# Optimization experiments

Hardware: AMD Instinct MI355X
Metric: run time of the kernel (lower is better)

Reference implementation:

```python
import jax, jax.numpy as jnp
import numpy as np

NFFT = 4_194_304
NMODES = 2
NTAPS = 101
GAMMA = 0.0016567  # [/W/m]
DZ = 80000.0       # [m]


def setup_inputs() -> dict:
    key = jax.random.key(0)
    k1, k2, k3 = jax.random.split(key, 3)
    xr = jax.random.normal(k1, (NFFT, NMODES), dtype=jnp.float32)
    xi = jax.random.normal(k2, (NFFT, NMODES), dtype=jnp.float32)
    # fconv1d kernel: [ntaps, in_features=Nmodes, out_features=Nmodes] (lecun_normal-ish scale)
    W = jax.random.normal(k3, (NTAPS, NMODES, NMODES), dtype=jnp.float32) / np.sqrt(NTAPS * NMODES)
    b = jnp.zeros((NMODES,), dtype=jnp.float32)
    power = jnp.zeros((1,), dtype=jnp.float32)  # 0 dBm
    return {"xr": xr, "xi": xi, "W": W, "b": b, "power": power}


def reference(xr, xi, W, b, power):
    # P = |x|^2, shape [Nfft, Nmodes]
    P = xr * xr + xi * xi
    # valid 1D conv over time: [Nfft, Nmodes] -> [Nfft - ntaps + 1, Nmodes]
    phi = jax.lax.conv_general_dilated(
        P[None],            # [1, Nfft, Nmodes]
        W,                  # [ntaps, in, out]
        window_strides=(1,),
        padding='VALID',
        dimension_numbers=('NWC', 'WIO', 'NWC'),
    )[0] + b                # [Nfft - ntaps + 1, Nmodes]

    nmodes = xr.shape[-1]
    scale = 0.001 * 10.0 ** (power[0] / 10.0) / nmodes  # dBm -> W, per mode
    n0 = NTAPS // 2
    x = (xr + 1j * xi)[n0:xr.shape[0] - n0]  # valid-conv aligned slice
    y = x * jnp.exp(-1j * phi * (GAMMA * scale * DZ))
    return y
```

## Files before the change

### kernel.cpp

```cpp
#include <hip/hip_runtime.h>
#include <hip/hip_bf16.h>

#define NFFT   4194304
#define NMODES 2
#define NTAPS  101
#define NVALID (NFFT - NTAPS + 1)
#define N0     (NTAPS / 2)

constexpr int BLOCK = 256;
constexpr int TILE  = 2048;
constexpr int NT    = (NVALID + TILE - 1) / TILE;
constexpr int WIN   = 2176;
constexpr int NCH   = WIN / 2;
constexpr int NM    = 15;
constexpr int TBW   = 272;

constexpr int OXA = 0;
constexpr int OXB = 4352;
constexpr int OPL = 8704;
constexpr int OBT = 10880;
constexpr int LWORDS = 11152;

typedef __attribute__((ext_vector_type(8)))  short short8;
typedef __attribute__((ext_vector_type(16))) float float16;

static __device__ __forceinline__ unsigned short f2bf(float x) {
    __hip_bfloat16 h = __float2bfloat16(x);
    return *reinterpret_cast<unsigned short*>(&h);
}
static __device__ __forceinline__ unsigned pk(float e0, float e1) {
    return (unsigned)f2bf(e0) | ((unsigned)f2bf(e1) << 16);
}
static __device__ __forceinline__ int swz(int s) {
    return s ^ (((s >> 5) & 7) << 2);
}
static __device__ __forceinline__ void gl16(const float4* g, unsigned* l) {
    __builtin_amdgcn_global_load_lds(
        (const __attribute__((address_space(1))) void*)g,
        (__attribute__((address_space(3))) void*)l, 16, 0, 0);
}

__global__ __launch_bounds__(BLOCK, 3) void nl_kernel(
    const float* __restrict__ xa,
    const float* __restrict__ xb,
    const float* __restrict__ W,  const float* __restrict__ b,
    const float* __restrict__ power, unsigned* __restrict__ out)
{
    __shared__ __align__(16) unsigned lds[LWORDS];
    unsigned* const xaR = lds + OXA;
    unsigned* const xbR = lds + OXB;
    unsigned* const Pl  = lds + OPL;
    unsigned* const Bt  = lds + OBT;

    const int tid  = threadIdx.x;
    const int lane = tid & 63;
    const int wid  = tid >> 6;
    const int colc = lane & 31;
    const int h    = lane >> 5;
    const int cs   = colc >> 1;
    const int o    = colc & 1;
    const int r    = colc;

    const int tile_start = blockIdx.x * TILE;
    const int ts2        = tile_start >> 1;

    const float4* __restrict__ xa4 = reinterpret_cast<const float4*>(xa);
    const float4* __restrict__ xb4 = reinterpret_cast<const float4*>(xb);
    #pragma unroll
    for (int k = 0; k < 4; ++k) {
        const int c  = tid + 256 * k;
        const int cc = min(ts2 + c, NFFT / 2 - 1);
        gl16(xa4 + cc, &xaR[4 * c]);
        gl16(xb4 + cc, &xbR[4 * c]);
    }
    if (tid < 64) {
        const int c  = tid + 1024;
        const int cc = min(ts2 + c, NFFT / 2 - 1);
        gl16(xa4 + cc, &xaR[4 * c]);
        gl16(xb4 + cc, &xbR[4 * c]);
    }

    __builtin_amdgcn_sched_barrier(0);

    {
        const float4* __restrict__ Wt = reinterpret_cast<const float4*>(W);
        #pragma unroll
        for (int idx = tid; idx < TBW; idx += BLOCK) {
            const int t  = (idx >> 1) - 15;
            const int oo = idx & 1;
            const bool ok = (unsigned)t <= 100u;
            const float4 w = Wt[ok ? t : 0];
            Bt[idx] = ok ? pk(oo ? w.y : w.x, oo ? w.w : w.z) : 0u;
        }
    }
    __syncthreads();

    #pragma unroll
    for (int k = 0; k < 5; ++k) {
        const int tp = tid + 256 * k;
        if (k < 4 || tp < NCH) {
            const float4 a = *reinterpret_cast<const float4*>(&xaR[4 * tp]);
            const float4 c = *reinterpret_cast<const float4*>(&xbR[4 * tp]);
            const int g = tile_start + 2 * tp;
            unsigned u0 = 0u, u1 = 0u;
            if (g < NFFT) {
                u0 = pk(a.x * a.x + c.x * c.x, a.y * a.y + c.y * c.y);
                u1 = pk(a.z * a.z + c.z * c.z, a.w * a.w + c.w * c.w);
            }
            *reinterpret_cast<uint2*>(&Pl[swz(2 * tp)]) = make_uint2(u0, u1);
        }
    }
    __syncthreads();

    const int cb    = wid * 512;
    const int bbase = ((4 * h - cs + 15) << 1) | o;
    float16 acc = {};
    uint4 areg[4];
    #pragma unroll
    for (int m = 0; m < 4; ++m)
        areg[m] = *reinterpret_cast<const uint4*>(&Pl[swz(cb + 16 * r + 8 * m + 4 * h)]);
    #pragma unroll
    for (int m = 0; m < NM; ++m) {
        uint4 bq;
        bq.x = Bt[bbase + 16 * m + 0];
        bq.y = Bt[bbase + 16 * m + 2];
        bq.z = Bt[bbase + 16 * m + 4];
        bq.w = Bt[bbase + 16 * m + 6];
        acc = __builtin_amdgcn_mfma_f32_32x32x16_bf16(
                  __builtin_bit_cast(short8, areg[m & 3]),
                  __builtin_bit_cast(short8, bq), acc, 0, 0, 0);
        if (m + 4 < NM)
            areg[m & 3] = *reinterpret_cast<const uint4*>(
                              &Pl[swz(cb + 16 * r + 8 * (m + 4) + 4 * h)]);
    }

    const float bo   = o ? b[1] : b[0];
    const float coef = 0.066268f * exp10f(power[0] * 0.1f);
    const float* __restrict__ xaF = reinterpret_cast<const float*>(xaR);
    const float* __restrict__ xbF = reinterpret_cast<const float*>(xbR);

    if (blockIdx.x != NT - 1) {
        #pragma unroll
        for (int j = 0; j < 16; ++j) {
            const int row = (j & 3) + 8 * (j >> 2) + 4 * h;
            const int lw  = 2 * (cb + 16 * row + cs + N0) + o;
            const float Ax = xaF[lw];
            const float Bx = xbF[lw];
            float sn, cn;
            __sincosf((acc[j] + bo) * coef, &sn, &cn);
            const int n = tile_start + cb + 16 * row + cs;
            __builtin_nontemporal_store(pk(Bx * cn - Ax * sn, Ax * cn + Bx * sn),
                                        &out[n * 2 + o]);
        }
    } else {
        #pragma unroll
        for (int j = 0; j < 16; ++j) {
            const int row = (j & 3) + 8 * (j >> 2) + 4 * h;
            const int n   = tile_start + cb + 16 * row + cs;
            if (n < NVALID) {
                const int lw  = 2 * (cb + 16 * row + cs + N0) + o;
                const float Ax = xaF[lw];
                const float Bx = xbF[lw];
                float sn, cn;
                __sincosf((acc[j] + bo) * coef, &sn, &cn);
                __builtin_nontemporal_store(pk(Bx * cn - Ax * sn, Ax * cn + Bx * sn),
                                            &out[n * 2 + o]);
            }
        }
    }
}

extern "C" void kernel_launch(void* const* d_in, const int* in_sizes, int n_in,
                              void* d_out, int out_size, void* d_ws, size_t ws_size,
                              hipStream_t stream) {
    const float* big[2] = {nullptr, nullptr};
    const float* W = nullptr; const float* b = nullptr; const float* power = nullptr;
    int nbig = 0;
    for (int i = 0; i < n_in; ++i) {
        const float* p = (const float*)d_in[i];
        const int sz = in_sizes[i];
        if (sz == NFFT * NMODES)       { if (nbig < 2) big[nbig++] = p; }
        else if (sz == NTAPS * NMODES * NMODES) { W = p; }
        else if (sz == NMODES)         { b = p; }
        else if (sz == 1)              { power = p; }
    }

    unsigned* out = (unsigned*)d_out;
    nl_kernel<<<NT, BLOCK, 0, stream>>>(big[0], big[1], W, b, power, out);
}
```

Baseline: 112.8 us.

## Switch to single-wave blocks with per-wave windows, removing block barriers

Each block is now one 64-lane wavefront covering a 512-sample tile with its own 640-sample window in LDS, replacing 4-wave blocks sharing a 2048-sample tile. This drops both __syncthreads barriers in favor of an explicit vmcnt wait, and cuts LDS per block so more blocks can be resident. In exchange the 101-tap halo is re-read for every 512 samples rather than every 2048, adding global read traffic, and the weight table is rebuilt four times as often.

```diff
diff --git a/kernel.cpp b/kernel.cpp
--- a/kernel.cpp
+++ b/kernel.cpp
@@ -7,19 +7,18 @@
 #define NVALID (NFFT - NTAPS + 1)
 #define N0     (NTAPS / 2)
 
-constexpr int BLOCK = 256;
-constexpr int TILE  = 2048;
+constexpr int BLOCK = 64;
+constexpr int TILE  = 512;
 constexpr int NT    = (NVALID + TILE - 1) / TILE;
-constexpr int WIN   = 2176;
+constexpr int WIN   = 640;
 constexpr int NCH   = WIN / 2;
 constexpr int NM    = 15;
 constexpr int TBW   = 272;
 
-constexpr int OXA = 0;
-constexpr int OXB = 4352;
-constexpr int OPL = 8704;
-constexpr int OBT = 10880;
-constexpr int LWORDS = 11152;
+constexpr int OXB = 1280;
+constexpr int OPL = 2560;
+constexpr int OBT = 3200;
+constexpr int LWORDS = 3472;
 
 typedef __attribute__((ext_vector_type(8)))  short short8;
 typedef __attribute__((ext_vector_type(16))) float float16;
@@ -40,85 +39,76 @@
         (__attribute__((address_space(3))) void*)l, 16, 0, 0);
 }
 
-__global__ __launch_bounds__(BLOCK, 3) void nl_kernel(
+__global__ __launch_bounds__(BLOCK, 4) void nl_kernel(
     const float* __restrict__ xa,
     const float* __restrict__ xb,
     const float* __restrict__ W,  const float* __restrict__ b,
     const float* __restrict__ power, unsigned* __restrict__ out)
 {
     __shared__ __align__(16) unsigned lds[LWORDS];
-    unsigned* const xaR = lds + OXA;
+    unsigned* const xaR = lds;
     unsigned* const xbR = lds + OXB;
     unsigned* const Pl  = lds + OPL;
     unsigned* const Bt  = lds + OBT;
 
-    const int tid  = threadIdx.x;
-    const int lane = tid & 63;
-    const int wid  = tid >> 6;
+    const int lane = threadIdx.x & 63;
     const int colc = lane & 31;
     const int h    = lane >> 5;
     const int cs   = colc >> 1;
     const int o    = colc & 1;
     const int r    = colc;
 
-    const int tile_start = blockIdx.x * TILE;
-    const int ts2        = tile_start >> 1;
+    const int wstart = blockIdx.x * TILE;
+    const int ts2    = wstart >> 1;
 
     const float4* __restrict__ xa4 = reinterpret_cast<const float4*>(xa);
     const float4* __restrict__ xb4 = reinterpret_cast<const float4*>(xb);
     #pragma unroll
-    for (int k = 0; k < 4; ++k) {
-        const int c  = tid + 256 * k;
-        const int cc = min(ts2 + c, NFFT / 2 - 1);
-        gl16(xa4 + cc, &xaR[4 * c]);
-        gl16(xb4 + cc, &xbR[4 * c]);
-    }
-    if (tid < 64) {
-        const int c  = tid + 1024;
+    for (int k = 0; k < 5; ++k) {
+        const int c  = lane + 64 * k;
         const int cc = min(ts2 + c, NFFT / 2 - 1);
         gl16(xa4 + cc, &xaR[4 * c]);
         gl16(xb4 + cc, &xbR[4 * c]);
     }
 
-    __builtin_amdgcn_sched_barrier(0);
-
     {
         const float4* __restrict__ Wt = reinterpret_cast<const float4*>(W);
         #pragma unroll
-        for (int idx = tid; idx < TBW; idx += BLOCK) {
-            const int t  = (idx >> 1) - 15;
-            const int oo = idx & 1;
-            const bool ok = (unsigned)t <= 100u;
-            const float4 w = Wt[ok ? t : 0];
-            Bt[idx] = ok ? pk(oo ? w.y : w.x, oo ? w.w : w.z) : 0u;
+        for (int k = 0; k < 5; ++k) {
+            const int idx = lane + 64 * k;
+            if (k < 4 || idx < TBW) {
+                const int t  = (idx >> 1) - 15;
+                const int oo = idx & 1;
+                const bool ok = (unsigned)t <= 100u;
+                const float4 w = Wt[ok ? t : 0];
+                Bt[idx] = ok ? pk(oo ? w.y : w.x, oo ? w.w : w.z) : 0u;
+            }
         }
     }
-    __syncthreads();
+
+    asm volatile("s_waitcnt vmcnt(0)" ::: "memory");
+    __builtin_amdgcn_sched_barrier(0);
 
     #pragma unroll
     for (int k = 0; k < 5; ++k) {
-        const int tp = tid + 256 * k;
-        if (k < 4 || tp < NCH) {
-            const float4 a = *reinterpret_cast<const float4*>(&xaR[4 * tp]);
-            const float4 c = *reinterpret_cast<const float4*>(&xbR[4 * tp]);
-            const int g = tile_start + 2 * tp;
-            unsigned u0 = 0u, u1 = 0u;
-            if (g < NFFT) {
-                u0 = pk(a.x * a.x + c.x * c.x, a.y * a.y + c.y * c.y);
-                u1 = pk(a.z * a.z + c.z * c.z, a.w * a.w + c.w * c.w);
-            }
-            *reinterpret_cast<uint2*>(&Pl[swz(2 * tp)]) = make_uint2(u0, u1);
+        const int tp = lane + 64 * k;
+        const float4 a = *reinterpret_cast<const float4*>(&xaR[4 * tp]);
+        const float4 c = *reinterpret_cast<const float4*>(&xbR[4 * tp]);
+        const int g = wstart + 2 * tp;
+        unsigned u0 = 0u, u1 = 0u;
+        if (g < NFFT) {
+            u0 = pk(a.x * a.x + c.x * c.x, a.y * a.y + c.y * c.y);
+            u1 = pk(a.z * a.z + c.z * c.z, a.w * a.w + c.w * c.w);
         }
+        *reinterpret_cast<uint2*>(&Pl[swz(2 * tp)]) = make_uint2(u0, u1);
     }
-    __syncthreads();
 
-    const int cb    = wid * 512;
     const int bbase = ((4 * h - cs + 15) << 1) | o;
     float16 acc = {};
     uint4 areg[4];
     #pragma unroll
     for (int m = 0; m < 4; ++m)
-        areg[m] = *reinterpret_cast<const uint4*>(&Pl[swz(cb + 16 * r + 8 * m + 4 * h)]);
+        areg[m] = *reinterpret_cast<const uint4*>(&Pl[swz(16 * r + 8 * m + 4 * h)]);
     #pragma unroll
     for (int m = 0; m < NM; ++m) {
         uint4 bq;
@@ -131,7 +121,7 @@
                   __builtin_bit_cast(short8, bq), acc, 0, 0, 0);
         if (m + 4 < NM)
             areg[m & 3] = *reinterpret_cast<const uint4*>(
-                              &Pl[swz(cb + 16 * r + 8 * (m + 4) + 4 * h)]);
+                              &Pl[swz(16 * r + 8 * (m + 4) + 4 * h)]);
     }
 
     const float bo   = o ? b[1] : b[0];
@@ -143,12 +133,12 @@
         #pragma unroll
         for (int j = 0; j < 16; ++j) {
             const int row = (j & 3) + 8 * (j >> 2) + 4 * h;
-            const int lw  = 2 * (cb + 16 * row + cs + N0) + o;
+            const int lw  = 2 * (16 * row + cs + N0) + o;
             const float Ax = xaF[lw];
             const float Bx = xbF[lw];
             float sn, cn;
             __sincosf((acc[j] + bo) * coef, &sn, &cn);
-            const int n = tile_start + cb + 16 * row + cs;
+            const int n = wstart + 16 * row + cs;
             __builtin_nontemporal_store(pk(Bx * cn - Ax * sn, Ax * cn + Bx * sn),
                                         &out[n * 2 + o]);
         }
@@ -156,9 +146,9 @@
         #pragma unroll
         for (int j = 0; j < 16; ++j) {
             const int row = (j & 3) + 8 * (j >> 2) + 4 * h;
-            const int n   = tile_start + cb + 16 * row + cs;
+            const int n   = wstart + 16 * row + cs;
             if (n < NVALID) {
-                const int lw  = 2 * (cb + 16 * row + cs + N0) + o;
+                const int lw  = 2 * (16 * row + cs + N0) + o;
                 const float Ax = xaF[lw];
                 const float Bx = xbF[lw];
                 float sn, cn;
```

Result: slower. 116.2 us (+3.0%).
